# Performance work log

Hardware: AMD Instinct MI355X
Metric: run time of the kernel (lower is better)

## Reference

```python
import jax, jax.numpy as jnp
import numpy as np

EPS = 1e-5

def _ln(x, g, b):
    mu = jnp.mean(x, axis=-1, keepdims=True)
    var = jnp.mean(jnp.square(x - mu), axis=-1, keepdims=True)
    return (x - mu) * jax.lax.rsqrt(var + EPS) * g + b

def setup_inputs() -> dict:
    key = jax.random.key(0)
    ks = jax.random.split(key, 12)
    B, N, CZ, CF, CP = 1, 512, 128, 384, 256
    s = 0.02
    return {
        'z': jax.random.normal(ks[0], (B, N, N, CZ), jnp.float32),
        'framepair_embed': jax.random.normal(ks[1], (B, N, N, CP), jnp.float32),
        'rigids_embed_flat': jax.random.normal(ks[2], (B, N, CF), jnp.float32),
        'rigids_to_res_idx': jax.random.randint(ks[3], (B, N), 0, N, dtype=jnp.int64),
        'rigids_mask': jnp.ones((B, N), jnp.float32),
        # nodepair_to_framepair_broadcast: LayerNorm(c_z) + Linear(c_z, c_framepair, bias=False)
        'ln_z_g': jnp.ones((CZ,), jnp.float32),
        'ln_z_b': jnp.zeros((CZ,), jnp.float32),
        'W_z': jax.random.normal(ks[4], (CZ, CP), jnp.float32) * s,
        # frame_ln + two bias-free broadcasts
        'ln_f_g': jnp.ones((CF,), jnp.float32),
        'ln_f_b': jnp.zeros((CF,), jnp.float32),
        'W_l': jax.random.normal(ks[5], (CF, CP), jnp.float32) * s,
        'W_m': jax.random.normal(ks[6], (CF, CP), jnp.float32) * s,
        # framepair_ffn: LN + Linear + ReLU + Linear + ReLU + Linear
        'ffn_ln_g': jnp.ones((CP,), jnp.float32),
        'ffn_ln_b': jnp.zeros((CP,), jnp.float32),
        'W1': jax.random.normal(ks[7], (CP, CP), jnp.float32) * s,
        'b1': jnp.zeros((CP,), jnp.float32),
        'W2': jax.random.normal(ks[8], (CP, CP), jnp.float32) * s,
        'b2': jnp.zeros((CP,), jnp.float32),
        'W3': jax.random.normal(ks[9], (CP, CP), jnp.float32) * s,
        'b3': jnp.zeros((CP,), jnp.float32),
    }

def reference(z, framepair_embed, rigids_embed_flat, rigids_to_res_idx, rigids_mask,
              ln_z_g, ln_z_b, W_z, ln_f_g, ln_f_b, W_l, W_m,
              ffn_ln_g, ffn_ln_b, W1, b1, W2, b2, W3, b3):
    # --- broadcast singles: row + column frame features into pair rep ---
    src = _ln(rigids_embed_flat, ln_f_g, ln_f_b)            # [B, N, CF]
    l = jnp.einsum('bnf,fp->bnp', src, W_l)                 # [B, N, CP]
    m = jnp.einsum('bnf,fp->bnp', src, W_m)
    fe = framepair_embed + l[:, :, None, :] + m[:, None, :, :]
    # --- broadcast pairs: irregular gather of residue-pair features ---
    ii = rigids_to_res_idx[0]                               # [N] (batch-0 indices, as in torch code)
    zb = z[:, ii[:, None], ii[None, :]]                     # [B, N, N, CZ]
    mk = rigids_mask[0]
    pair_mask = (mk[:, None] * mk[None, :])[None, :, :, None]
    zb = zb * pair_mask
    fe = fe + jnp.einsum('bijc,cp->bijp', _ln(zb, ln_z_g, ln_z_b), W_z)
    # --- framepair FFN with residual ---
    h = _ln(fe, ffn_ln_g, ffn_ln_b)
    h = jax.nn.relu(jnp.einsum('bijp,pq->bijq', h, W1) + b1)
    h = jax.nn.relu(jnp.einsum('bijp,pq->bijq', h, W2) + b2)
    fe = fe + jnp.einsum('bijp,pq->bijq', h, W3) + b3
    return fe
```

## Files before the change

kernel.cpp:

```cpp
#include <hip/hip_runtime.h>

#define NN 512
#define CZv 128
#define CFv 384
#define CPv 256
#define ROWS 64

typedef __attribute__((ext_vector_type(8))) short s16x8;
typedef __attribute__((ext_vector_type(4))) short s16x4;
typedef __attribute__((ext_vector_type(4))) float f32x4;

__device__ __forceinline__ unsigned short f2bf(float f) {
  unsigned int u = __builtin_bit_cast(unsigned int, f);
  u = (u + 0x7FFFu + ((u >> 16) & 1u)) >> 16;
  return (unsigned short)u;
}
__device__ __forceinline__ float bf2f(unsigned short h) {
  unsigned int u = ((unsigned int)h) << 16;
  return __builtin_bit_cast(float, u);
}

__global__ void pack_w(const float* __restrict__ W, short* __restrict__ Wf, int total) {
  int o = blockIdx.x * 256 + threadIdx.x;
  if (o >= total) return;
  int e = o & 7;
  int l = (o >> 3) & 63;
  int mt = (o >> 9) & 15;
  int kk = o >> 13;
  int k = kk * 32 + (l >> 4) * 8 + e;
  int p = mt * 16 + (l & 15);
  Wf[o] = (short)f2bf(W[k * 256 + p]);
}

__global__ __launch_bounds__(256) void lm_kernel(
    const float* __restrict__ rf, const float* __restrict__ g, const float* __restrict__ b,
    const float* __restrict__ Wl, const float* __restrict__ Wm,
    float* __restrict__ lout, float* __restrict__ mout) {
  __shared__ float S[8][CFv];
  const int tid = threadIdx.x;
  const int w = tid >> 6;
  const int lane = tid & 63;
  for (int rr = 0; rr < 2; ++rr) {
    int r = blockIdx.x * 8 + w * 2 + rr;
    const float* x = rf + (long)r * CFv;
    float v[6];
    float s1 = 0.f, s2 = 0.f;
#pragma unroll
    for (int q = 0; q < 6; ++q) {
      v[q] = x[lane + q * 64];
      s1 += v[q];
      s2 += v[q] * v[q];
    }
#pragma unroll
    for (int off = 1; off < 64; off <<= 1) {
      s1 += __shfl_xor(s1, off, 64);
      s2 += __shfl_xor(s2, off, 64);
    }
    float mu = s1 * (1.f / CFv);
    float va = s2 * (1.f / CFv) - mu * mu;
    float rs = rsqrtf(va + 1e-5f);
#pragma unroll
    for (int q = 0; q < 6; ++q) {
      int k = lane + q * 64;
      S[w * 2 + rr][k] = (v[q] - mu) * rs * g[k] + b[k];
    }
  }
  __syncthreads();
  float accl[8], accm[8];
#pragma unroll
  for (int r = 0; r < 8; ++r) { accl[r] = 0.f; accm[r] = 0.f; }
  for (int k = 0; k < CFv; ++k) {
    float wl = Wl[k * CPv + tid];
    float wm = Wm[k * CPv + tid];
#pragma unroll
    for (int r = 0; r < 8; ++r) {
      accl[r] += S[r][k] * wl;
      accm[r] += S[r][k] * wm;
    }
  }
#pragma unroll
  for (int r = 0; r < 8; ++r) {
    long rg = blockIdx.x * 8 + r;
    lout[rg * CPv + tid] = accl[r];
    mout[rg * CPv + tid] = accm[r];
  }
}

__global__ __launch_bounds__(512, 4) void fused_main(
    const float* __restrict__ z, const float* __restrict__ fpe,
    const int* __restrict__ idx, const float* __restrict__ msk,
    const float* __restrict__ lnzg, const float* __restrict__ lnzb,
    const float* __restrict__ ffng, const float* __restrict__ ffnb,
    const float* __restrict__ b1p, const float* __restrict__ b2p, const float* __restrict__ b3p,
    const float* __restrict__ lws, const float* __restrict__ mws,
    const short* __restrict__ Wzf, const short* __restrict__ W1f,
    const short* __restrict__ W2f, const short* __restrict__ W3f,
    float* __restrict__ out) {
  __shared__ __align__(16) char X[ROWS * CPv * 2];
  __shared__ __align__(16) char Xres[ROWS * CPv * 2];
  __shared__ float SS[8][ROWS];
  __shared__ float SQ[8][ROWS];

  const int tid = threadIdx.x;
  const int w = tid >> 6;
  const int lane = tid & 63;
  const int l15 = lane & 15;
  const int lg = lane >> 4;
  const int mt0 = 2 * w;

  const int b = blockIdx.x;
  const int tile = (b & 7) * 512 + (b >> 3);
  const int i = tile >> 3;
  const int j0 = (tile & 7) * ROWS;
  const int r0 = tile * ROWS;

  f32x4 fe[4][2];
  {
    f32x4 lb[2];
    const float* lr = lws + (long)i * CPv;
#pragma unroll
    for (int mi = 0; mi < 2; ++mi)
      lb[mi] = *(const f32x4*)(lr + (mt0 + mi) * 16 + lg * 4);
#pragma unroll
    for (int nt = 0; nt < 4; ++nt) {
      const int row = nt * 16 + l15;
      const long rg = (long)r0 + row;
      const float* fpr = fpe + rg * CPv;
      const float* mr = mws + (long)(j0 + row) * CPv;
#pragma unroll
      for (int mi = 0; mi < 2; ++mi) {
        const int c0 = (mt0 + mi) * 16 + lg * 4;
        f32x4 a = *(const f32x4*)(fpr + c0);
        f32x4 mb = *(const f32x4*)(mr + c0);
        fe[nt][mi] = a + lb[mi] + mb;
      }
    }
  }

  {
    const int row = w * 8 + (lane & 7);
    const int seg = (lane >> 3) * 16;
    const int j = j0 + row;
    const int ia = idx[i];
    const int jb = idx[j];
    const float pm = msk[i] * msk[j];
    const float* zr = z + ((long)ia * NN + jb) * CZv + seg;
    f32x4 zv[4];
    float s1 = 0.f, s2 = 0.f;
#pragma unroll
    for (int q = 0; q < 4; ++q) {
      zv[q] = *(const f32x4*)(zr + q * 4);
#pragma unroll
      for (int e = 0; e < 4; ++e) {
        float v = zv[q][e] * pm;
        zv[q][e] = v;
        s1 += v;
        s2 += v * v;
      }
    }
    s1 += __shfl_xor(s1, 8, 64);
    s1 += __shfl_xor(s1, 16, 64);
    s1 += __shfl_xor(s1, 32, 64);
    s2 += __shfl_xor(s2, 8, 64);
    s2 += __shfl_xor(s2, 16, 64);
    s2 += __shfl_xor(s2, 32, 64);
    float mu = s1 * (1.f / CZv);
    float va = s2 * (1.f / CZv) - mu * mu;
    float rs = rsqrtf(va + 1e-5f);
    const int swz = (row & 7) << 4;
#pragma unroll
    for (int h = 0; h < 2; ++h) {
      const f32x4 g0 = *(const f32x4*)(lnzg + seg + h * 8);
      const f32x4 g1 = *(const f32x4*)(lnzg + seg + h * 8 + 4);
      const f32x4 q0 = *(const f32x4*)(lnzb + seg + h * 8);
      const f32x4 q1 = *(const f32x4*)(lnzb + seg + h * 8 + 4);
      s16x8 hv;
#pragma unroll
      for (int e = 0; e < 4; ++e) {
        hv[e] = (short)f2bf((zv[h * 2][e] - mu) * rs * g0[e] + q0[e]);
        hv[4 + e] = (short)f2bf((zv[h * 2 + 1][e] - mu) * rs * g1[e] + q1[e]);
      }
      int off = (row * 256 + seg * 2 + h * 16) ^ swz;
      *(s16x8*)(X + off) = hv;
    }
  }
  __syncthreads();

  {
    const s16x8* Wp = (const s16x8*)Wzf;
    auto ldw = [&](int kk, s16x8(&a)[2]) {
      a[0] = Wp[(kk * 16 + mt0 + 0) * 64 + lane];
      a[1] = Wp[(kk * 16 + mt0 + 1) * 64 + lane];
    };
    auto step = [&](int kk, const s16x8(&a)[2]) {
#pragma unroll
      for (int nt = 0; nt < 4; ++nt) {
        const int row = nt * 16 + l15;
        int off = (row * 256 + kk * 64 + lg * 16) ^ ((row & 7) << 4);
        s16x8 bfr = *(const s16x8*)(X + off);
#pragma unroll
        for (int mi = 0; mi < 2; ++mi)
          fe[nt][mi] = __builtin_amdgcn_mfma_f32_16x16x32_bf16(a[mi], bfr, fe[nt][mi], 0, 0, 0);
      }
    };
    s16x8 afA[2], afB[2], afC[2];
    ldw(0, afA);
    ldw(1, afB);
    __builtin_amdgcn_s_setprio(1);
    ldw(2, afC);
    step(0, afA);
    ldw(3, afA);
    step(1, afB);
    step(2, afC);
    step(3, afA);
    __builtin_amdgcn_s_setprio(0);
  }

  float mu4[4], rs4[4];
  {
#pragma unroll
    for (int nt = 0; nt < 4; ++nt) {
      float s = 0.f, q = 0.f;
#pragma unroll
      for (int mi = 0; mi < 2; ++mi)
#pragma unroll
        for (int e = 0; e < 4; ++e) {
          float v = fe[nt][mi][e];
          s += v;
          q += v * v;
        }
      s += __shfl_xor(s, 16, 64);
      s += __shfl_xor(s, 32, 64);
      q += __shfl_xor(q, 16, 64);
      q += __shfl_xor(q, 32, 64);
      if (lane < 16) {
        SS[w][nt * 16 + lane] = s;
        SQ[w][nt * 16 + lane] = q;
      }
    }
    __syncthreads();
#pragma unroll
    for (int nt = 0; nt < 4; ++nt) {
      const int row = nt * 16 + l15;
      float ts = 0.f, tq = 0.f;
#pragma unroll
      for (int ww = 0; ww < 8; ++ww) {
        ts += SS[ww][row];
        tq += SQ[ww][row];
      }
      float mu = ts * (1.f / CPv);
      float va = tq * (1.f / CPv) - mu * mu;
      mu4[nt] = mu;
      rs4[nt] = rsqrtf(va + 1e-5f);
    }
  }

#pragma unroll
  for (int mi = 0; mi < 2; ++mi) {
    const int c0 = (mt0 + mi) * 16 + lg * 4;
    const f32x4 g4 = *(const f32x4*)(ffng + c0);
    const f32x4 b4 = *(const f32x4*)(ffnb + c0);
#pragma unroll
    for (int nt = 0; nt < 4; ++nt) {
      const int row = nt * 16 + l15;
      const int swz = (row & 7) << 4;
      s16x4 hv, fv;
#pragma unroll
      for (int e = 0; e < 4; ++e) {
        float v = fe[nt][mi][e];
        hv[e] = (short)f2bf((v - mu4[nt]) * rs4[nt] * g4[e] + b4[e]);
        fv[e] = (short)f2bf(v);
      }
      int off = (row * 512 + c0 * 2) ^ swz;
      *(s16x4*)(X + off) = hv;
      *(s16x4*)(Xres + off) = fv;
    }
  }
  __syncthreads();

  auto ffn_gemm = [&](const short* Wf, f32x4(&acc)[4][2]) {
    const s16x8* Wp = (const s16x8*)Wf;
    auto ldw = [&](int kk, s16x8(&a)[2]) {
      a[0] = Wp[(kk * 16 + mt0 + 0) * 64 + lane];
      a[1] = Wp[(kk * 16 + mt0 + 1) * 64 + lane];
    };
    auto step = [&](int kk, const s16x8(&a)[2]) {
#pragma unroll
      for (int nt = 0; nt < 4; ++nt) {
        const int row = nt * 16 + l15;
        int off = (row * 512 + kk * 64 + lg * 16) ^ ((row & 7) << 4);
        s16x8 bfr = *(const s16x8*)(X + off);
#pragma unroll
        for (int mi = 0; mi < 2; ++mi)
          acc[nt][mi] = __builtin_amdgcn_mfma_f32_16x16x32_bf16(a[mi], bfr, acc[nt][mi], 0, 0, 0);
      }
    };
    s16x8 afA[2], afB[2], afC[2];
    ldw(0, afA);
    ldw(1, afB);
    __builtin_amdgcn_s_setprio(1);
    ldw(2, afC);
    step(0, afA);
    ldw(3, afA);
    step(1, afB);
    ldw(4, afB);
    step(2, afC);
    ldw(5, afC);
    step(3, afA);
    ldw(6, afA);
    step(4, afB);
    ldw(7, afB);
    step(5, afC);
    step(6, afA);
    step(7, afB);
    __builtin_amdgcn_s_setprio(0);
  };

  auto write_relu = [&](f32x4(&acc)[4][2]) {
#pragma unroll
    for (int nt = 0; nt < 4; ++nt) {
      const int row = nt * 16 + l15;
      const int swz = (row & 7) << 4;
#pragma unroll
      for (int mi = 0; mi < 2; ++mi) {
        const int c0 = (mt0 + mi) * 16 + lg * 4;
        s16x4 hv;
#pragma unroll
        for (int e = 0; e < 4; ++e) {
          float v = acc[nt][mi][e];
          v = v > 0.f ? v : 0.f;
          hv[e] = (short)f2bf(v);
        }
        int off = (row * 512 + c0 * 2) ^ swz;
        *(s16x4*)(X + off) = hv;
      }
    }
  };

  f32x4 hacc[4][2];
#pragma unroll
  for (int mi = 0; mi < 2; ++mi) {
    const f32x4 bini = *(const f32x4*)(b1p + (mt0 + mi) * 16 + lg * 4);
#pragma unroll
    for (int nt = 0; nt < 4; ++nt) hacc[nt][mi] = bini;
  }
  ffn_gemm(W1f, hacc);
  __syncthreads();
  write_relu(hacc);
  __syncthreads();

#pragma unroll
  for (int mi = 0; mi < 2; ++mi) {
    const f32x4 bini = *(const f32x4*)(b2p + (mt0 + mi) * 16 + lg * 4);
#pragma unroll
    for (int nt = 0; nt < 4; ++nt) hacc[nt][mi] = bini;
  }
  ffn_gemm(W2f, hacc);
  __syncthreads();
  write_relu(hacc);
  __syncthreads();

#pragma unroll
  for (int mi = 0; mi < 2; ++mi) {
    const f32x4 b34 = *(const f32x4*)(b3p + (mt0 + mi) * 16 + lg * 4);
    const int c0 = (mt0 + mi) * 16 + lg * 4;
#pragma unroll
    for (int nt = 0; nt < 4; ++nt) {
      const int row = nt * 16 + l15;
      const int swz = (row & 7) << 4;
      int off = (row * 512 + c0 * 2) ^ swz;
      s16x4 fv = *(const s16x4*)(Xres + off);
#pragma unroll
      for (int e = 0; e < 4; ++e)
        hacc[nt][mi][e] = bf2f((unsigned short)fv[e]) + b34[e];
    }
  }
  ffn_gemm(W3f, hacc);
#pragma unroll
  for (int nt = 0; nt < 4; ++nt) {
    const long rg = (long)r0 + nt * 16 + l15;
#pragma unroll
    for (int mi = 0; mi < 2; ++mi) {
      const int c0 = (mt0 + mi) * 16 + lg * 4;
      *(f32x4*)(out + rg * CPv + c0) = hacc[nt][mi];
    }
  }
}

extern "C" void kernel_launch(void* const* d_in, const int* in_sizes, int n_in,
                              void* d_out, int out_size, void* d_ws, size_t ws_size,
                              hipStream_t stream) {
  const float* z = (const float*)d_in[0];
  const float* fpe = (const float*)d_in[1];
  const float* rf = (const float*)d_in[2];
  const int* idx = (const int*)d_in[3];
  const float* msk = (const float*)d_in[4];
  const float* lnzg = (const float*)d_in[5];
  const float* lnzb = (const float*)d_in[6];
  const float* Wz = (const float*)d_in[7];
  const float* lnfg = (const float*)d_in[8];
  const float* lnfb = (const float*)d_in[9];
  const float* Wl = (const float*)d_in[10];
  const float* Wm = (const float*)d_in[11];
  const float* ffng = (const float*)d_in[12];
  const float* ffnb = (const float*)d_in[13];
  const float* W1 = (const float*)d_in[14];
  const float* b1 = (const float*)d_in[15];
  const float* W2 = (const float*)d_in[16];
  const float* b2 = (const float*)d_in[17];
  const float* W3 = (const float*)d_in[18];
  const float* b3 = (const float*)d_in[19];
  float* out = (float*)d_out;

  char* ws = (char*)d_ws;
  float* lws = (float*)ws;
  float* mws = (float*)(ws + 512 * 1024);
  short* Wzf = (short*)(ws + 1024 * 1024);
  short* W1f = (short*)(ws + 1024 * 1024 + 64 * 1024);
  short* W2f = (short*)(ws + 1024 * 1024 + 192 * 1024);
  short* W3f = (short*)(ws + 1024 * 1024 + 320 * 1024);

  pack_w<<<128, 256, 0, stream>>>(Wz, Wzf, 128 * 256);
  pack_w<<<256, 256, 0, stream>>>(W1, W1f, 256 * 256);
  pack_w<<<256, 256, 0, stream>>>(W2, W2f, 256 * 256);
  pack_w<<<256, 256, 0, stream>>>(W3, W3f, 256 * 256);
  lm_kernel<<<64, 256, 0, stream>>>(rf, lnfg, lnfb, Wl, Wm, lws, mws);
  fused_main<<<4096, 512, 0, stream>>>(z, fpe, idx, msk, lnzg, lnzb, ffng, ffnb,
                                       b1, b2, b3, lws, mws, Wzf, W1f, W2f, W3f, out);
}
```

Before: 312.5 us.

## Ping-pong FFN LDS buffers, stash fp32 residual in output, merge weight packing

```diff
diff --git a/kernel.cpp b/kernel.cpp
--- a/kernel.cpp
+++ b/kernel.cpp
@@ -15,21 +15,26 @@
   u = (u + 0x7FFFu + ((u >> 16) & 1u)) >> 16;
   return (unsigned short)u;
 }
-__device__ __forceinline__ float bf2f(unsigned short h) {
-  unsigned int u = ((unsigned int)h) << 16;
-  return __builtin_bit_cast(float, u);
-}
-
-__global__ void pack_w(const float* __restrict__ W, short* __restrict__ Wf, int total) {
+
+__global__ void pack_all(const float* __restrict__ Wz, const float* __restrict__ W1,
+                         const float* __restrict__ W2, const float* __restrict__ W3,
+                         short* __restrict__ Wzf, short* __restrict__ W1f,
+                         short* __restrict__ W2f, short* __restrict__ W3f) {
   int o = blockIdx.x * 256 + threadIdx.x;
-  if (o >= total) return;
-  int e = o & 7;
-  int l = (o >> 3) & 63;
-  int mt = (o >> 9) & 15;
-  int kk = o >> 13;
+  const float* W;
+  short* Wf;
+  int lo;
+  if (o < 32768) { W = Wz; Wf = Wzf; lo = o; }
+  else if (o < 98304) { W = W1; Wf = W1f; lo = o - 32768; }
+  else if (o < 163840) { W = W2; Wf = W2f; lo = o - 98304; }
+  else { W = W3; Wf = W3f; lo = o - 163840; }
+  int e = lo & 7;
+  int l = (lo >> 3) & 63;
+  int mt = (lo >> 9) & 15;
+  int kk = lo >> 13;
   int k = kk * 32 + (l >> 4) * 8 + e;
   int p = mt * 16 + (l & 15);
-  Wf[o] = (short)f2bf(W[k * 256 + p]);
+  Wf[lo] = (short)f2bf(W[k * 256 + p]);
 }
 
 __global__ __launch_bounds__(256) void lm_kernel(
@@ -97,9 +102,9 @@
     const short* __restrict__ W2f, const short* __restrict__ W3f,
     float* __restrict__ out) {
   __shared__ __align__(16) char X[ROWS * CPv * 2];
-  __shared__ __align__(16) char Xres[ROWS * CPv * 2];
-  __shared__ float SS[8][ROWS];
-  __shared__ float SQ[8][ROWS];
+  __shared__ __align__(16) char X2[ROWS * CPv * 2];
+  float* SS = (float*)X2;
+  float* SQ = (float*)(X2 + 2048);
 
   const int tid = threadIdx.x;
   const int w = tid >> 6;
@@ -234,8 +239,8 @@
       q += __shfl_xor(q, 16, 64);
       q += __shfl_xor(q, 32, 64);
       if (lane < 16) {
-        SS[w][nt * 16 + lane] = s;
-        SQ[w][nt * 16 + lane] = q;
+        SS[w * 64 + nt * 16 + lane] = s;
+        SQ[w * 64 + nt * 16 + lane] = q;
       }
     }
     __syncthreads();
@@ -245,8 +250,8 @@
       float ts = 0.f, tq = 0.f;
 #pragma unroll
       for (int ww = 0; ww < 8; ++ww) {
-        ts += SS[ww][row];
-        tq += SQ[ww][row];
+        ts += SS[ww * 64 + row];
+        tq += SQ[ww * 64 + row];
       }
       float mu = ts * (1.f / CPv);
       float va = tq * (1.f / CPv) - mu * mu;
@@ -264,21 +269,30 @@
     for (int nt = 0; nt < 4; ++nt) {
       const int row = nt * 16 + l15;
       const int swz = (row & 7) << 4;
-      s16x4 hv, fv;
+      s16x4 hv;
 #pragma unroll
       for (int e = 0; e < 4; ++e) {
         float v = fe[nt][mi][e];
         hv[e] = (short)f2bf((v - mu4[nt]) * rs4[nt] * g4[e] + b4[e]);
-        fv[e] = (short)f2bf(v);
       }
       int off = (row * 512 + c0 * 2) ^ swz;
       *(s16x4*)(X + off) = hv;
-      *(s16x4*)(Xres + off) = fv;
+    }
+  }
+
+#pragma unroll
+  for (int mi = 0; mi < 2; ++mi) {
+    const int c0 = (mt0 + mi) * 16 + lg * 4;
+    const f32x4 b34 = *(const f32x4*)(b3p + c0);
+#pragma unroll
+    for (int nt = 0; nt < 4; ++nt) {
+      const long rg = (long)r0 + nt * 16 + l15;
+      *(f32x4*)(out + rg * CPv + c0) = fe[nt][mi] + b34;
     }
   }
   __syncthreads();
 
-  auto ffn_gemm = [&](const short* Wf, f32x4(&acc)[4][2]) {
+  auto ffn_gemm = [&](const short* Wf, const char* Xb, f32x4(&acc)[4][2]) {
     const s16x8* Wp = (const s16x8*)Wf;
     auto ldw = [&](int kk, s16x8(&a)[2]) {
       a[0] = Wp[(kk * 16 + mt0 + 0) * 64 + lane];
@@ -289,7 +303,7 @@
       for (int nt = 0; nt < 4; ++nt) {
         const int row = nt * 16 + l15;
         int off = (row * 512 + kk * 64 + lg * 16) ^ ((row & 7) << 4);
-        s16x8 bfr = *(const s16x8*)(X + off);
+        s16x8 bfr = *(const s16x8*)(Xb + off);
 #pragma unroll
         for (int mi = 0; mi < 2; ++mi)
           acc[nt][mi] = __builtin_amdgcn_mfma_f32_16x16x32_bf16(a[mi], bfr, acc[nt][mi], 0, 0, 0);
@@ -316,7 +330,7 @@
     __builtin_amdgcn_s_setprio(0);
   };
 
-  auto write_relu = [&](f32x4(&acc)[4][2]) {
+  auto write_relu = [&](char* Xb, f32x4(&acc)[4][2]) {
 #pragma unroll
     for (int nt = 0; nt < 4; ++nt) {
       const int row = nt * 16 + l15;
@@ -332,7 +346,7 @@
           hv[e] = (short)f2bf(v);
         }
         int off = (row * 512 + c0 * 2) ^ swz;
-        *(s16x4*)(X + off) = hv;
+        *(s16x4*)(Xb + off) = hv;
       }
     }
   };
@@ -344,9 +358,8 @@
 #pragma unroll
     for (int nt = 0; nt < 4; ++nt) hacc[nt][mi] = bini;
   }
-  ffn_gemm(W1f, hacc);
-  __syncthreads();
-  write_relu(hacc);
+  ffn_gemm(W1f, X, hacc);
+  write_relu(X2, hacc);
   __syncthreads();
 
 #pragma unroll
@@ -355,27 +368,20 @@
 #pragma unroll
     for (int nt = 0; nt < 4; ++nt) hacc[nt][mi] = bini;
   }
-  ffn_gemm(W2f, hacc);
+  ffn_gemm(W2f, X2, hacc);
+  write_relu(X, hacc);
   __syncthreads();
-  write_relu(hacc);
-  __syncthreads();
-
-#pragma unroll
-  for (int mi = 0; mi < 2; ++mi) {
-    const f32x4 b34 = *(const f32x4*)(b3p + (mt0 + mi) * 16 + lg * 4);
-    const int c0 = (mt0 + mi) * 16 + lg * 4;
-#pragma unroll
-    for (int nt = 0; nt < 4; ++nt) {
-      const int row = nt * 16 + l15;
-      const int swz = (row & 7) << 4;
-      int off = (row * 512 + c0 * 2) ^ swz;
-      s16x4 fv = *(const s16x4*)(Xres + off);
-#pragma unroll
-      for (int e = 0; e < 4; ++e)
-        hacc[nt][mi][e] = bf2f((unsigned short)fv[e]) + b34[e];
-    }
-  }
-  ffn_gemm(W3f, hacc);
+
+#pragma unroll
+  for (int nt = 0; nt < 4; ++nt) {
+    const long rg = (long)r0 + nt * 16 + l15;
+#pragma unroll
+    for (int mi = 0; mi < 2; ++mi) {
+      const int c0 = (mt0 + mi) * 16 + lg * 4;
+      hacc[nt][mi] = *(const f32x4*)(out + rg * CPv + c0);
+    }
+  }
+  ffn_gemm(W3f, X, hacc);
 #pragma unroll
   for (int nt = 0; nt < 4; ++nt) {
     const long rg = (long)r0 + nt * 16 + l15;
@@ -420,10 +426,7 @@
   short* W2f = (short*)(ws + 1024 * 1024 + 192 * 1024);
   short* W3f = (short*)(ws + 1024 * 1024 + 320 * 1024);
 
-  pack_w<<<128, 256, 0, stream>>>(Wz, Wzf, 128 * 256);
-  pack_w<<<256, 256, 0, stream>>>(W1, W1f, 256 * 256);
-  pack_w<<<256, 256, 0, stream>>>(W2, W2f, 256 * 256);
-  pack_w<<<256, 256, 0, stream>>>(W3, W3f, 256 * 256);
+  pack_all<<<896, 256, 0, stream>>>(Wz, W1, W2, W3, Wzf, W1f, W2f, W3f);
   lm_kernel<<<64, 256, 0, stream>>>(rf, lnfg, lnfb, Wl, Wm, lws, mws);
   fused_main<<<4096, 512, 0, stream>>>(z, fpe, idx, msk, lnzg, lnzb, ffng, ffnb,
                                        b1, b2, b3, lws, mws, Wzf, W1f, W2f, W3f, out);
```

Result: slower. 364.0 us (+16.5%).
